# Performance work log

Hardware: AMD Instinct MI355X
Metric: run time of the kernel (lower is better)

The kernel has to match this reference:

```python
import jax, jax.numpy as jnp
import numpy as np

B, N, D = 16, 32768, 256
E, H, K, T = 512, 8, 512, 16  # text_embed_dim, nhead, top_k, num_defect_tokens
LN_EPS = 1e-5


def setup_inputs() -> dict:
    key = jax.random.key(0)
    ks = jax.random.split(key, 8)
    sc = 0.02
    return {
        "per_point_features": jax.random.normal(ks[0], (B, N, D), jnp.float32),
        "outlier_scores": jax.random.normal(ks[1], (B, N, 1), jnp.float32),
        "proj_w": jax.random.normal(ks[2], (E, D), jnp.float32) * sc,
        "proj_b": jnp.zeros((E,), jnp.float32),
        "in_proj_w": jax.random.normal(ks[3], (3 * E, E), jnp.float32) * sc,
        "in_proj_b": jnp.zeros((3 * E,), jnp.float32),
        "out_proj_w": jax.random.normal(ks[4], (E, E), jnp.float32) * sc,
        "out_proj_b": jnp.zeros((E,), jnp.float32),
        "ln_g": jnp.ones((E,), jnp.float32),
        "ln_b": jnp.zeros((E,), jnp.float32),
        "ffn_w": jax.random.normal(ks[5], (E, E), jnp.float32) * sc,
        "ffn_b": jnp.zeros((E,), jnp.float32),
    }


def _layernorm(x, g, b):
    mu = jnp.mean(x, axis=-1, keepdims=True)
    var = jnp.mean(jnp.square(x - mu), axis=-1, keepdims=True)
    return (x - mu) * jax.lax.rsqrt(var + LN_EPS) * g + b


def reference(per_point_features, outlier_scores, proj_w, proj_b,
              in_proj_w, in_proj_b, out_proj_w, out_proj_b,
              ln_g, ln_b, ffn_w, ffn_b):
    # top-k select + gather
    scores = outlier_scores[..., 0]                       # [B, N]
    _, idx = jax.lax.top_k(scores, K)                     # [B, K]
    feats = jnp.take_along_axis(per_point_features, idx[:, :, None], axis=1)  # [B, K, D]
    # linear projection to text embed dim
    x = feats @ proj_w.T + proj_b                         # [B, K, E]
    # multi-head self-attention (torch nn.MultiheadAttention semantics)
    qkv = x @ in_proj_w.T + in_proj_b                     # [B, K, 3E]
    q, k, v = jnp.split(qkv, 3, axis=-1)
    dh = E // H
    q = q.reshape(B, K, H, dh)
    k = k.reshape(B, K, H, dh)
    v = v.reshape(B, K, H, dh)
    logits = jnp.einsum("bqhd,bkhd->bhqk", q, k) / np.sqrt(dh).astype(np.float32)
    attn = jax.nn.softmax(logits, axis=-1)
    o = jnp.einsum("bhqk,bkhd->bqhd", attn, v).reshape(B, K, E)
    o = o @ out_proj_w.T + out_proj_b
    # residual + layernorm
    y = _layernorm(x + o, ln_g, ln_b)
    # FFN (linear + exact GELU) with residual
    y = y + jax.nn.gelu(y @ ffn_w.T + ffn_b, approximate=False)
    return y[:, :T, :]                                    # [B, T, E]
```

## Files before the change

### kernel.cpp

```cpp
#include <hip/hip_runtime.h>
#include <hip/hip_bf16.h>
#include <math.h>

#define PB 16
#define PN 32768
#define PD 256
#define PE 512
#define PH 8
#define PK 512
#define PT 16
#define DH 64

typedef __attribute__((ext_vector_type(8))) short bf16x8;
typedef __attribute__((ext_vector_type(4))) float f32x4;

__global__ __launch_bounds__(512) void topk_kernel(const float* __restrict__ scores,
                                                   int* __restrict__ sorted_idx) {
    const int b = blockIdx.x;
    const int tid = threadIdx.x;
    const int NT = 512;
    const float* s = scores + (size_t)b * PN;

    __shared__ unsigned int hist[256];
    __shared__ unsigned int sh_prefix;
    __shared__ int sh_remaining;
    __shared__ unsigned int sh_cnt_gt, sh_cnt_eq;
    __shared__ unsigned long long comp[PK];
    __shared__ unsigned int eq_idx[PK];

    unsigned int prefix = 0;
    int remaining = PK;
    for (int shift = 24; shift >= 0; shift -= 8) {
        for (int i = tid; i < 256; i += NT) hist[i] = 0;
        __syncthreads();
        for (int i = tid; i < PN; i += NT) {
            unsigned int u = __float_as_uint(s[i]);
            u = (u & 0x80000000u) ? ~u : (u | 0x80000000u);
            bool ok = (shift == 24) || ((u >> (shift + 8)) == prefix);
            if (ok) atomicAdd(&hist[(u >> shift) & 0xFFu], 1u);
        }
        __syncthreads();
        if (tid == 0) {
            int cum = 0;
            int d = 255;
            for (; d >= 0; --d) {
                cum += (int)hist[d];
                if (cum >= remaining) break;
            }
            sh_remaining = remaining - (cum - (int)hist[d]);
            sh_prefix = (prefix << 8) | (unsigned)d;
        }
        __syncthreads();
        prefix = sh_prefix;
        remaining = sh_remaining;
        __syncthreads();
    }
    const unsigned int TKEY = prefix;

    if (tid == 0) { sh_cnt_gt = 0; sh_cnt_eq = 0; }
    __syncthreads();
    for (int i = tid; i < PN; i += NT) {
        unsigned int u = __float_as_uint(s[i]);
        u = (u & 0x80000000u) ? ~u : (u | 0x80000000u);
        if (u > TKEY) {
            unsigned p = atomicAdd(&sh_cnt_gt, 1u);
            comp[p] = ((unsigned long long)u << 32) | (unsigned int)(~(unsigned)i);
        } else if (u == TKEY) {
            unsigned p = atomicAdd(&sh_cnt_eq, 1u);
            if (p < PK) eq_idx[p] = (unsigned)i;
        }
    }
    __syncthreads();
    const int cnt_gt = (int)sh_cnt_gt;
    const int need_eq = PK - cnt_gt;
    const int ec = (int)sh_cnt_eq < PK ? (int)sh_cnt_eq : PK;
    if (tid == 0) {
        for (int j = 0; j < need_eq; ++j) {
            unsigned mv = 0xFFFFFFFFu; int mb = 0;
            for (int i2 = 0; i2 < ec; ++i2)
                if (eq_idx[i2] < mv) { mv = eq_idx[i2]; mb = i2; }
            comp[cnt_gt + j] = ((unsigned long long)TKEY << 32) | (unsigned int)(~mv);
            eq_idx[mb] = 0xFFFFFFFFu;
        }
    }
    __syncthreads();

    for (unsigned ksz = 2; ksz <= PK; ksz <<= 1) {
        for (unsigned j = ksz >> 1; j > 0; j >>= 1) {
            unsigned i = (unsigned)tid;
            unsigned ixj = i ^ j;
            if (ixj > i && i < PK) {
                unsigned long long a = comp[i], c = comp[ixj];
                bool sw = ((i & ksz) == 0) ? (a < c) : (a > c);
                if (sw) { comp[i] = c; comp[ixj] = a; }
            }
            __syncthreads();
        }
    }
    if (tid < PK)
        sorted_idx[b * PK + tid] = (int)(~(unsigned int)(comp[tid] & 0xFFFFFFFFull));
}

__global__ void gather_cast_kernel(const float* __restrict__ feats,
                                   const int* __restrict__ sidx,
                                   __hip_bfloat16* __restrict__ Ag) {
    const int row = blockIdx.x;
    const int b = row >> 9;
    const int src = sidx[row];
    const float* p = feats + ((size_t)b * PN + (size_t)src) * PD;
    __hip_bfloat16* q = Ag + (size_t)row * PD;
    for (int i = threadIdx.x; i < PD; i += blockDim.x)
        q[i] = __float2bfloat16(p[i]);
}

__global__ void cast_f32_bf16_kernel(const float* __restrict__ src,
                                     __hip_bfloat16* __restrict__ dst, int n) {
    int i = blockIdx.x * blockDim.x + threadIdx.x;
    if (i < n) dst[i] = __float2bfloat16(src[i]);
}

__global__ __launch_bounds__(256) void gemm_bt_bf16_kernel(
    const short* __restrict__ A, const short* __restrict__ Bm,
    const float* __restrict__ bias,
    float* __restrict__ C32, __hip_bfloat16* __restrict__ C16,
    int M, int N, int Kd) {
    const int tid = threadIdx.x;
    const int wave = tid >> 6;
    const int lane = tid & 63;
    const int m0 = blockIdx.x * 128 + (wave >> 1) * 64;
    const int n0 = blockIdx.y * 128 + (wave & 1) * 64;
    const int mrow = lane & 15;
    const int quad = lane >> 4;

    f32x4 acc[4][4] = {};
    for (int k0 = 0; k0 < Kd; k0 += 32) {
        const int kk = k0 + quad * 8;
        bf16x8 a[4], bf[4];
#pragma unroll
        for (int i = 0; i < 4; ++i)
            a[i] = *(const bf16x8*)(A + (size_t)(m0 + i * 16 + mrow) * Kd + kk);
#pragma unroll
        for (int i = 0; i < 4; ++i)
            bf[i] = *(const bf16x8*)(Bm + (size_t)(n0 + i * 16 + mrow) * Kd + kk);
#pragma unroll
        for (int i = 0; i < 4; ++i)
#pragma unroll
            for (int j = 0; j < 4; ++j)
                acc[i][j] = __builtin_amdgcn_mfma_f32_16x16x32_bf16(a[i], bf[j], acc[i][j], 0, 0, 0);
    }
#pragma unroll
    for (int i = 0; i < 4; ++i)
#pragma unroll
        for (int j = 0; j < 4; ++j)
#pragma unroll
            for (int r = 0; r < 4; ++r) {
                int row = m0 + i * 16 + quad * 4 + r;
                int col = n0 + j * 16 + mrow;
                float v = acc[i][j][r] + bias[col];
                if (C32) C32[(size_t)row * N + col] = v;
                if (C16) C16[(size_t)row * N + col] = __float2bfloat16(v);
            }
}

__global__ void extract_xq_kernel(const float* __restrict__ x, float* __restrict__ xq) {
    const int r = blockIdx.x;
    const int b = r >> 4, t = r & 15;
    const float* src = x + ((size_t)b * PK + t) * PE;
    float* dst = xq + (size_t)r * PE;
    for (int i = threadIdx.x; i < PE; i += blockDim.x) dst[i] = src[i];
}

__global__ __launch_bounds__(256) void sgemm_bt_kernel(
    const float* __restrict__ A, const float* __restrict__ Bm,
    const float* __restrict__ bias, float* __restrict__ C,
    int M, int N, int Kd) {
    __shared__ float As[32][33];
    __shared__ float Bs[32][33];
    const int tid = threadIdx.x;
    const int m0 = blockIdx.x * 32, n0 = blockIdx.y * 32;
    const int tx = tid & 15, ty = tid >> 4;
    float acc00 = 0, acc01 = 0, acc10 = 0, acc11 = 0;
    for (int k0 = 0; k0 < Kd; k0 += 32) {
        for (int e = tid; e < 1024; e += 256) {
            int r = e >> 5, c = e & 31;
            As[r][c] = A[(size_t)(m0 + r) * Kd + k0 + c];
            Bs[r][c] = Bm[(size_t)(n0 + r) * Kd + k0 + c];
        }
        __syncthreads();
#pragma unroll
        for (int kk = 0; kk < 32; ++kk) {
            float a0 = As[ty * 2][kk], a1 = As[ty * 2 + 1][kk];
            float b0 = Bs[tx * 2][kk], b1 = Bs[tx * 2 + 1][kk];
            acc00 += a0 * b0; acc01 += a0 * b1;
            acc10 += a1 * b0; acc11 += a1 * b1;
        }
        __syncthreads();
    }
    float bc0 = bias[n0 + tx * 2], bc1 = bias[n0 + tx * 2 + 1];
    C[(size_t)(m0 + ty * 2) * N + n0 + tx * 2]         = acc00 + bc0;
    C[(size_t)(m0 + ty * 2) * N + n0 + tx * 2 + 1]     = acc01 + bc1;
    C[(size_t)(m0 + ty * 2 + 1) * N + n0 + tx * 2]     = acc10 + bc0;
    C[(size_t)(m0 + ty * 2 + 1) * N + n0 + tx * 2 + 1] = acc11 + bc1;
}

__global__ __launch_bounds__(256) void attn_kernel(
    const float* __restrict__ qb, const __hip_bfloat16* __restrict__ kv,
    float* __restrict__ ob) {
    const int bh = blockIdx.x;
    const int b = bh >> 3, h = bh & 7;
    const int tid = threadIdx.x;
    __shared__ float qs[PT][DH + 1];
    __shared__ float ls[PT][PK + 1];

    for (int i = tid; i < PT * DH; i += 256) {
        int t = i >> 6, d = i & 63;
        qs[t][d] = qb[(size_t)(b * PT + t) * PE + h * DH + d];
    }
    __syncthreads();

    const int t = tid >> 4;
    const int ko = tid & 15;
    for (int k = ko; k < PK; k += 16) {
        const __hip_bfloat16* kp = kv + (size_t)(b * PK + k) * (2 * PE) + h * DH;
        float acc = 0;
#pragma unroll 8
        for (int d = 0; d < DH; ++d) acc += qs[t][d] * __bfloat162float(kp[d]);
        ls[t][k] = acc * 0.125f;
    }
    float m = -1e30f;
    for (int k = ko; k < PK; k += 16) m = fmaxf(m, ls[t][k]);
#pragma unroll
    for (int s = 8; s >= 1; s >>= 1) m = fmaxf(m, __shfl_xor(m, s, 16));
    float sum = 0;
    for (int k = ko; k < PK; k += 16) {
        float e = __expf(ls[t][k] - m);
        ls[t][k] = e;
        sum += e;
    }
#pragma unroll
    for (int s = 8; s >= 1; s >>= 1) sum += __shfl_xor(sum, s, 16);
    const float inv = 1.0f / sum;

    const int dv = tid & 15;
    float o0 = 0, o1 = 0, o2 = 0, o3 = 0;
    for (int k = 0; k < PK; ++k) {
        float w = ls[t][k];
        const __hip_bfloat16* vp = kv + (size_t)(b * PK + k) * (2 * PE) + PE + h * DH;
        o0 += w * __bfloat162float(vp[dv]);
        o1 += w * __bfloat162float(vp[dv + 16]);
        o2 += w * __bfloat162float(vp[dv + 32]);
        o3 += w * __bfloat162float(vp[dv + 48]);
    }
    float* orow = ob + (size_t)(b * PT + t) * PE + h * DH;
    orow[dv]      = o0 * inv;
    orow[dv + 16] = o1 * inv;
    orow[dv + 32] = o2 * inv;
    orow[dv + 48] = o3 * inv;
}

__global__ __launch_bounds__(256) void ln_kernel(
    const float* __restrict__ xq, const float* __restrict__ o2,
    const float* __restrict__ g, const float* __restrict__ bb,
    float* __restrict__ y) {
    const int r = blockIdx.x;
    const int tid = threadIdx.x;
    __shared__ float red[4], red2[4];
    float v0 = xq[(size_t)r * PE + tid] + o2[(size_t)r * PE + tid];
    float v1 = xq[(size_t)r * PE + 256 + tid] + o2[(size_t)r * PE + 256 + tid];
    float s = v0 + v1;
#pragma unroll
    for (int sh = 32; sh >= 1; sh >>= 1) s += __shfl_xor(s, sh, 64);
    if ((tid & 63) == 0) red[tid >> 6] = s;
    __syncthreads();
    float mean = (red[0] + red[1] + red[2] + red[3]) * (1.0f / 512.0f);
    float d0 = v0 - mean, d1 = v1 - mean;
    float sq = d0 * d0 + d1 * d1;
#pragma unroll
    for (int sh = 32; sh >= 1; sh >>= 1) sq += __shfl_xor(sq, sh, 64);
    if ((tid & 63) == 0) red2[tid >> 6] = sq;
    __syncthreads();
    float var = (red2[0] + red2[1] + red2[2] + red2[3]) * (1.0f / 512.0f);
    float rs = rsqrtf(var + 1e-5f);
    y[(size_t)r * PE + tid]       = d0 * rs * g[tid] + bb[tid];
    y[(size_t)r * PE + 256 + tid] = d1 * rs * g[tid + 256] + bb[tid + 256];
}

__global__ void gelu_res_kernel(const float* __restrict__ y,
                                const float* __restrict__ z,
                                float* __restrict__ out, int n) {
    int i = blockIdx.x * blockDim.x + threadIdx.x;
    if (i < n) {
        float zz = z[i];
        float gl = 0.5f * zz * (1.0f + erff(zz * 0.7071067811865475f));
        out[i] = y[i] + gl;
    }
}

extern "C" void kernel_launch(void* const* d_in, const int* in_sizes, int n_in,
                              void* d_out, int out_size, void* d_ws, size_t ws_size,
                              hipStream_t stream) {
    const float* feats  = (const float*)d_in[0];
    const float* scores = (const float*)d_in[1];
    const float* proj_w = (const float*)d_in[2];
    const float* proj_b = (const float*)d_in[3];
    const float* in_w   = (const float*)d_in[4];
    const float* in_b   = (const float*)d_in[5];
    const float* out_w  = (const float*)d_in[6];
    const float* out_b  = (const float*)d_in[7];
    const float* ln_g   = (const float*)d_in[8];
    const float* ln_b   = (const float*)d_in[9];
    const float* ffn_w  = (const float*)d_in[10];
    const float* ffn_b  = (const float*)d_in[11];
    float* out = (float*)d_out;

    char* p = (char*)d_ws;
    auto alloc = [&](size_t bytes) {
        void* r = (void*)p;
        p += (bytes + 255) & ~(size_t)255;
        return r;
    };
    int* sidx             = (int*)alloc((size_t)PB * PK * 4);
    __hip_bfloat16* Ag    = (__hip_bfloat16*)alloc((size_t)PB * PK * PD * 2);
    __hip_bfloat16* Wp16  = (__hip_bfloat16*)alloc((size_t)PE * PD * 2);
    __hip_bfloat16* Wkv16 = (__hip_bfloat16*)alloc((size_t)2 * PE * PE * 2);
    float* x32            = (float*)alloc((size_t)PB * PK * PE * 4);
    __hip_bfloat16* x16   = (__hip_bfloat16*)alloc((size_t)PB * PK * PE * 2);
    __hip_bfloat16* kv16  = (__hip_bfloat16*)alloc((size_t)PB * PK * 2 * PE * 2);
    float* xq             = (float*)alloc((size_t)PB * PT * PE * 4);
    float* qb             = (float*)alloc((size_t)PB * PT * PE * 4);
    float* ob             = (float*)alloc((size_t)PB * PT * PE * 4);
    float* o2             = (float*)alloc((size_t)PB * PT * PE * 4);
    float* yb             = (float*)alloc((size_t)PB * PT * PE * 4);
    float* zb             = (float*)alloc((size_t)PB * PT * PE * 4);
    if ((size_t)(p - (char*)d_ws) > ws_size) return;

    topk_kernel<<<PB, 512, 0, stream>>>(scores, sidx);
    gather_cast_kernel<<<PB * PK, 64, 0, stream>>>(feats, sidx, Ag);
    cast_f32_bf16_kernel<<<(PE * PD + 255) / 256, 256, 0, stream>>>(proj_w, Wp16, PE * PD);
    cast_f32_bf16_kernel<<<(2 * PE * PE + 255) / 256, 256, 0, stream>>>(in_w + (size_t)PE * PE, Wkv16, 2 * PE * PE);
    gemm_bt_bf16_kernel<<<dim3(64, 4), 256, 0, stream>>>(
        (const short*)Ag, (const short*)Wp16, proj_b, x32, x16, PB * PK, PE, PD);
    gemm_bt_bf16_kernel<<<dim3(64, 8), 256, 0, stream>>>(
        (const short*)x16, (const short*)Wkv16, in_b + PE, nullptr, kv16,
        PB * PK, 2 * PE, PE);
    extract_xq_kernel<<<PB * PT, 256, 0, stream>>>(x32, xq);
    sgemm_bt_kernel<<<dim3(8, 16), 256, 0, stream>>>(xq, in_w, in_b, qb, PB * PT, PE, PE);
    attn_kernel<<<PB * PH, 256, 0, stream>>>(qb, kv16, ob);
    sgemm_bt_kernel<<<dim3(8, 16), 256, 0, stream>>>(ob, out_w, out_b, o2, PB * PT, PE, PE);
    ln_kernel<<<PB * PT, 256, 0, stream>>>(xq, o2, ln_g, ln_b, yb);
    sgemm_bt_kernel<<<dim3(8, 16), 256, 0, stream>>>(yb, ffn_w, ffn_b, zb, PB * PT, PE, PE);
    gelu_res_kernel<<<(PB * PT * PE + 255) / 256, 256, 0, stream>>>(yb, zb, out, PB * PT * PE);
}
```

Before: 966.1 us.

## Vectorize loads, fuse casts, xq extraction and GELU epilogue, drop fp32 x buffer

Top-k histogram and selection passes now read scores as float4. The gather now uses one wave per row with float4 loads, and the two weight casts are merged into one vectorized kernel. The projection GEMM writes the first 16 token rows straight to xq instead of storing a full fp32 x and extracting it later. GELU plus residual moves into the FFN sgemm epilogue, and the attention kernel uses vectorized bf16 loads. Together these cut launches and memory traffic, with the main cost likely in the top-k kernel, which runs with only 16 blocks.

```diff
diff --git a/kernel.cpp b/kernel.cpp
--- a/kernel.cpp
+++ b/kernel.cpp
@@ -14,6 +14,14 @@
 typedef __attribute__((ext_vector_type(8))) short bf16x8;
 typedef __attribute__((ext_vector_type(4))) float f32x4;
 
+__device__ __forceinline__ unsigned short f2bf(float f) {
+    __hip_bfloat16 h = __float2bfloat16(f);
+    return *(unsigned short*)&h;
+}
+__device__ __forceinline__ float b2f(unsigned short u) {
+    return __uint_as_float(((unsigned int)u) << 16);
+}
+
 __global__ __launch_bounds__(512) void topk_kernel(const float* __restrict__ scores,
                                                    int* __restrict__ sorted_idx) {
     const int b = blockIdx.x;
@@ -33,11 +41,16 @@
     for (int shift = 24; shift >= 0; shift -= 8) {
         for (int i = tid; i < 256; i += NT) hist[i] = 0;
         __syncthreads();
-        for (int i = tid; i < PN; i += NT) {
-            unsigned int u = __float_as_uint(s[i]);
-            u = (u & 0x80000000u) ? ~u : (u | 0x80000000u);
-            bool ok = (shift == 24) || ((u >> (shift + 8)) == prefix);
-            if (ok) atomicAdd(&hist[(u >> shift) & 0xFFu], 1u);
+        for (int i = tid * 4; i < PN; i += NT * 4) {
+            float4 f = *(const float4*)(s + i);
+            const float* fp = (const float*)&f;
+#pragma unroll
+            for (int j = 0; j < 4; ++j) {
+                unsigned int u = __float_as_uint(fp[j]);
+                u = (u & 0x80000000u) ? ~u : (u | 0x80000000u);
+                bool ok = (shift == 24) || ((u >> (shift + 8)) == prefix);
+                if (ok) atomicAdd(&hist[(u >> shift) & 0xFFu], 1u);
+            }
         }
         __syncthreads();
         if (tid == 0) {
@@ -59,15 +72,20 @@
 
     if (tid == 0) { sh_cnt_gt = 0; sh_cnt_eq = 0; }
     __syncthreads();
-    for (int i = tid; i < PN; i += NT) {
-        unsigned int u = __float_as_uint(s[i]);
-        u = (u & 0x80000000u) ? ~u : (u | 0x80000000u);
-        if (u > TKEY) {
-            unsigned p = atomicAdd(&sh_cnt_gt, 1u);
-            comp[p] = ((unsigned long long)u << 32) | (unsigned int)(~(unsigned)i);
-        } else if (u == TKEY) {
-            unsigned p = atomicAdd(&sh_cnt_eq, 1u);
-            if (p < PK) eq_idx[p] = (unsigned)i;
+    for (int i = tid * 4; i < PN; i += NT * 4) {
+        float4 f = *(const float4*)(s + i);
+        const float* fp = (const float*)&f;
+#pragma unroll
+        for (int j = 0; j < 4; ++j) {
+            unsigned int u = __float_as_uint(fp[j]);
+            u = (u & 0x80000000u) ? ~u : (u | 0x80000000u);
+            if (u > TKEY) {
+                unsigned p = atomicAdd(&sh_cnt_gt, 1u);
+                comp[p] = ((unsigned long long)u << 32) | (unsigned int)(~(unsigned)(i + j));
+            } else if (u == TKEY) {
+                unsigned p = atomicAdd(&sh_cnt_eq, 1u);
+                if (p < PK) eq_idx[p] = (unsigned)(i + j);
+            }
         }
     }
     __syncthreads();
@@ -101,28 +119,41 @@
         sorted_idx[b * PK + tid] = (int)(~(unsigned int)(comp[tid] & 0xFFFFFFFFull));
 }
 
-__global__ void gather_cast_kernel(const float* __restrict__ feats,
-                                   const int* __restrict__ sidx,
-                                   __hip_bfloat16* __restrict__ Ag) {
-    const int row = blockIdx.x;
+__global__ __launch_bounds__(256) void gather_cast_kernel(const float* __restrict__ feats,
+                                                          const int* __restrict__ sidx,
+                                                          __hip_bfloat16* __restrict__ Ag) {
+    const int row = blockIdx.x * 4 + (threadIdx.x >> 6);
+    const int lane = threadIdx.x & 63;
     const int b = row >> 9;
     const int src = sidx[row];
-    const float* p = feats + ((size_t)b * PN + (size_t)src) * PD;
-    __hip_bfloat16* q = Ag + (size_t)row * PD;
-    for (int i = threadIdx.x; i < PD; i += blockDim.x)
-        q[i] = __float2bfloat16(p[i]);
-}
-
-__global__ void cast_f32_bf16_kernel(const float* __restrict__ src,
-                                     __hip_bfloat16* __restrict__ dst, int n) {
-    int i = blockIdx.x * blockDim.x + threadIdx.x;
-    if (i < n) dst[i] = __float2bfloat16(src[i]);
+    float4 f = *(const float4*)(feats + ((size_t)b * PN + (size_t)src) * PD + lane * 4);
+    ushort4 u;
+    u.x = f2bf(f.x); u.y = f2bf(f.y); u.z = f2bf(f.z); u.w = f2bf(f.w);
+    *(ushort4*)((unsigned short*)Ag + (size_t)row * PD + lane * 4) = u;
+}
+
+__global__ __launch_bounds__(256) void cast_weights_kernel(
+    const float* __restrict__ proj_w, const float* __restrict__ kv_w,
+    __hip_bfloat16* __restrict__ Wp16, __hip_bfloat16* __restrict__ Wkv16) {
+    const int n1 = PE * PD / 4;
+    const int n2 = 2 * PE * PE / 4;
+    int i = blockIdx.x * 256 + threadIdx.x;
+    const float4* src;
+    unsigned short* dst;
+    int off;
+    if (i < n1) { src = (const float4*)proj_w; dst = (unsigned short*)Wp16; off = i; }
+    else if (i < n1 + n2) { src = (const float4*)kv_w; dst = (unsigned short*)Wkv16; off = i - n1; }
+    else return;
+    float4 f = src[off];
+    ushort4 u;
+    u.x = f2bf(f.x); u.y = f2bf(f.y); u.z = f2bf(f.z); u.w = f2bf(f.w);
+    *(ushort4*)(dst + (size_t)off * 4) = u;
 }
 
 __global__ __launch_bounds__(256) void gemm_bt_bf16_kernel(
     const short* __restrict__ A, const short* __restrict__ Bm,
     const float* __restrict__ bias,
-    float* __restrict__ C32, __hip_bfloat16* __restrict__ C16,
+    __hip_bfloat16* __restrict__ C16, float* __restrict__ Xq,
     int M, int N, int Kd) {
     const int tid = threadIdx.x;
     const int wave = tid >> 6;
@@ -157,23 +188,22 @@
                 int row = m0 + i * 16 + quad * 4 + r;
                 int col = n0 + j * 16 + mrow;
                 float v = acc[i][j][r] + bias[col];
-                if (C32) C32[(size_t)row * N + col] = v;
-                if (C16) C16[(size_t)row * N + col] = __float2bfloat16(v);
-            }
-}
-
-__global__ void extract_xq_kernel(const float* __restrict__ x, float* __restrict__ xq) {
-    const int r = blockIdx.x;
-    const int b = r >> 4, t = r & 15;
-    const float* src = x + ((size_t)b * PK + t) * PE;
-    float* dst = xq + (size_t)r * PE;
-    for (int i = threadIdx.x; i < PE; i += blockDim.x) dst[i] = src[i];
+                if (C16) {
+                    __hip_bfloat16 hv = __float2bfloat16(v);
+                    ((__hip_bfloat16*)C16)[(size_t)row * N + col] = hv;
+                }
+                if (Xq) {
+                    int t = row & (PK - 1);
+                    if (t < PT)
+                        Xq[((size_t)(row >> 9) * PT + t) * N + col] = v;
+                }
+            }
 }
 
 __global__ __launch_bounds__(256) void sgemm_bt_kernel(
     const float* __restrict__ A, const float* __restrict__ Bm,
-    const float* __restrict__ bias, float* __restrict__ C,
-    int M, int N, int Kd) {
+    const float* __restrict__ bias, const float* __restrict__ resid,
+    float* __restrict__ C, int M, int N, int Kd) {
     __shared__ float As[32][33];
     __shared__ float Bs[32][33];
     const int tid = threadIdx.x;
@@ -197,10 +227,17 @@
         __syncthreads();
     }
     float bc0 = bias[n0 + tx * 2], bc1 = bias[n0 + tx * 2 + 1];
-    C[(size_t)(m0 + ty * 2) * N + n0 + tx * 2]         = acc00 + bc0;
-    C[(size_t)(m0 + ty * 2) * N + n0 + tx * 2 + 1]     = acc01 + bc1;
-    C[(size_t)(m0 + ty * 2 + 1) * N + n0 + tx * 2]     = acc10 + bc0;
-    C[(size_t)(m0 + ty * 2 + 1) * N + n0 + tx * 2 + 1] = acc11 + bc1;
+    float v00 = acc00 + bc0, v01 = acc01 + bc1, v10 = acc10 + bc0, v11 = acc11 + bc1;
+    size_t i00 = (size_t)(m0 + ty * 2) * N + n0 + tx * 2;
+    size_t i10 = (size_t)(m0 + ty * 2 + 1) * N + n0 + tx * 2;
+    if (resid) {
+        v00 = resid[i00]     + 0.5f * v00 * (1.0f + erff(v00 * 0.7071067811865475f));
+        v01 = resid[i00 + 1] + 0.5f * v01 * (1.0f + erff(v01 * 0.7071067811865475f));
+        v10 = resid[i10]     + 0.5f * v10 * (1.0f + erff(v10 * 0.7071067811865475f));
+        v11 = resid[i10 + 1] + 0.5f * v11 * (1.0f + erff(v11 * 0.7071067811865475f));
+    }
+    C[i00] = v00; C[i00 + 1] = v01;
+    C[i10] = v10; C[i10 + 1] = v11;
 }
 
 __global__ __launch_bounds__(256) void attn_kernel(
@@ -209,22 +246,29 @@
     const int bh = blockIdx.x;
     const int b = bh >> 3, h = bh & 7;
     const int tid = threadIdx.x;
-    __shared__ float qs[PT][DH + 1];
+    __shared__ float qs[PT][DH + 4];
     __shared__ float ls[PT][PK + 1];
 
-    for (int i = tid; i < PT * DH; i += 256) {
-        int t = i >> 6, d = i & 63;
-        qs[t][d] = qb[(size_t)(b * PT + t) * PE + h * DH + d];
+    {
+        int i4 = tid * 4;
+        int t = i4 >> 6, d = i4 & 63;
+        float4 f = *(const float4*)(qb + (size_t)(b * PT + t) * PE + h * DH + d);
+        qs[t][d] = f.x; qs[t][d + 1] = f.y; qs[t][d + 2] = f.z; qs[t][d + 3] = f.w;
     }
     __syncthreads();
 
     const int t = tid >> 4;
     const int ko = tid & 15;
     for (int k = ko; k < PK; k += 16) {
-        const __hip_bfloat16* kp = kv + (size_t)(b * PK + k) * (2 * PE) + h * DH;
+        const ushort4* kp = (const ushort4*)((const unsigned short*)kv +
+                             (size_t)(b * PK + k) * (2 * PE) + h * DH);
         float acc = 0;
-#pragma unroll 8
-        for (int d = 0; d < DH; ++d) acc += qs[t][d] * __bfloat162float(kp[d]);
+#pragma unroll
+        for (int c = 0; c < 16; ++c) {
+            ushort4 vv = kp[c];
+            acc += qs[t][c * 4 + 0] * b2f(vv.x) + qs[t][c * 4 + 1] * b2f(vv.y)
+                 + qs[t][c * 4 + 2] * b2f(vv.z) + qs[t][c * 4 + 3] * b2f(vv.w);
+        }
         ls[t][k] = acc * 0.125f;
     }
     float m = -1e30f;
@@ -241,21 +285,19 @@
     for (int s = 8; s >= 1; s >>= 1) sum += __shfl_xor(sum, s, 16);
     const float inv = 1.0f / sum;
 
-    const int dv = tid & 15;
+    const int d0 = (tid & 15) * 4;
+    const unsigned short* vbase = (const unsigned short*)kv +
+                                  (size_t)(b * PK) * (2 * PE) + PE + h * DH + d0;
     float o0 = 0, o1 = 0, o2 = 0, o3 = 0;
+#pragma unroll 4
     for (int k = 0; k < PK; ++k) {
         float w = ls[t][k];
-        const __hip_bfloat16* vp = kv + (size_t)(b * PK + k) * (2 * PE) + PE + h * DH;
-        o0 += w * __bfloat162float(vp[dv]);
-        o1 += w * __bfloat162float(vp[dv + 16]);
-        o2 += w * __bfloat162float(vp[dv + 32]);
-        o3 += w * __bfloat162float(vp[dv + 48]);
-    }
-    float* orow = ob + (size_t)(b * PT + t) * PE + h * DH;
-    orow[dv]      = o0 * inv;
-    orow[dv + 16] = o1 * inv;
-    orow[dv + 32] = o2 * inv;
-    orow[dv + 48] = o3 * inv;
+        ushort4 vv = *(const ushort4*)(vbase + (size_t)k * (2 * PE));
+        o0 += w * b2f(vv.x); o1 += w * b2f(vv.y);
+        o2 += w * b2f(vv.z); o3 += w * b2f(vv.w);
+    }
+    float4 o; o.x = o0 * inv; o.y = o1 * inv; o.z = o2 * inv; o.w = o3 * inv;
+    *(float4*)(ob + (size_t)(b * PT + t) * PE + h * DH + d0) = o;
 }
 
 __global__ __launch_bounds__(256) void ln_kernel(
@@ -283,17 +325,6 @@
     float rs = rsqrtf(var + 1e-5f);
     y[(size_t)r * PE + tid]       = d0 * rs * g[tid] + bb[tid];
     y[(size_t)r * PE + 256 + tid] = d1 * rs * g[tid + 256] + bb[tid + 256];
-}
-
-__global__ void gelu_res_kernel(const float* __restrict__ y,
-                                const float* __restrict__ z,
-                                float* __restrict__ out, int n) {
-    int i = blockIdx.x * blockDim.x + threadIdx.x;
-    if (i < n) {
-        float zz = z[i];
-        float gl = 0.5f * zz * (1.0f + erff(zz * 0.7071067811865475f));
-        out[i] = y[i] + gl;
-    }
 }
 
 extern "C" void kernel_launch(void* const* d_in, const int* in_sizes, int n_in,
@@ -323,7 +354,6 @@
     __hip_bfloat16* Ag    = (__hip_bfloat16*)alloc((size_t)PB * PK * PD * 2);
     __hip_bfloat16* Wp16  = (__hip_bfloat16*)alloc((size_t)PE * PD * 2);
     __hip_bfloat16* Wkv16 = (__hip_bfloat16*)alloc((size_t)2 * PE * PE * 2);
-    float* x32            = (float*)alloc((size_t)PB * PK * PE * 4);
     __hip_bfloat16* x16   = (__hip_bfloat16*)alloc((size_t)PB * PK * PE * 2);
     __hip_bfloat16* kv16  = (__hip_bfloat16*)alloc((size_t)PB * PK * 2 * PE * 2);
     float* xq             = (float*)alloc((size_t)PB * PT * PE * 4);
@@ -331,23 +361,23 @@
     float* ob             = (float*)alloc((size_t)PB * PT * PE * 4);
     float* o2             = (float*)alloc((size_t)PB * PT * PE * 4);
     float* yb             = (float*)alloc((size_t)PB * PT * PE * 4);
-    float* zb             = (float*)alloc((size_t)PB * PT * PE * 4);
     if ((size_t)(p - (char*)d_ws) > ws_size) return;
 
     topk_kernel<<<PB, 512, 0, stream>>>(scores, sidx);
-    gather_cast_kernel<<<PB * PK, 64, 0, stream>>>(feats, sidx, Ag);
-    cast_f32_bf16_kernel<<<(PE * PD + 255) / 256, 256, 0, stream>>>(proj_w, Wp16, PE * PD);
-    cast_f32_bf16_kernel<<<(2 * PE * PE + 255) / 256, 256, 0, stream>>>(in_w + (size_t)PE * PE, Wkv16, 2 * PE * PE);
+    gather_cast_kernel<<<PB * PK / 4, 256, 0, stream>>>(feats, sidx, Ag);
+    {
+        int nvec = (PE * PD + 2 * PE * PE) / 4;
+        cast_weights_kernel<<<(nvec + 255) / 256, 256, 0, stream>>>(
+            proj_w, in_w + (size_t)PE * PE, Wp16, Wkv16);
+    }
     gemm_bt_bf16_kernel<<<dim3(64, 4), 256, 0, stream>>>(
-        (const short*)Ag, (const short*)Wp16, proj_b, x32, x16, PB * PK, PE, PD);
+        (const short*)Ag, (const short*)Wp16, proj_b, x16, xq, PB * PK, PE, PD);
     gemm_bt_bf16_kernel<<<dim3(64, 8), 256, 0, stream>>>(
-        (const short*)x16, (const short*)Wkv16, in_b + PE, nullptr, kv16,
+        (const short*)x16, (const short*)Wkv16, in_b + PE, kv16, nullptr,
         PB * PK, 2 * PE, PE);
-    extract_xq_kernel<<<PB * PT, 256, 0, stream>>>(x32, xq);
-    sgemm_bt_kernel<<<dim3(8, 16), 256, 0, stream>>>(xq, in_w, in_b, qb, PB * PT, PE, PE);
+    sgemm_bt_kernel<<<dim3(8, 16), 256, 0, stream>>>(xq, in_w, in_b, nullptr, qb, PB * PT, PE, PE);
     attn_kernel<<<PB * PH, 256, 0, stream>>>(qb, kv16, ob);
-    sgemm_bt_kernel<<<dim3(8, 16), 256, 0, stream>>>(ob, out_w, out_b, o2, PB * PT, PE, PE);
+    sgemm_bt_kernel<<<dim3(8, 16), 256, 0, stream>>>(ob, out_w, out_b, nullptr, o2, PB * PT, PE, PE);
     ln_kernel<<<PB * PT, 256, 0, stream>>>(xq, o2, ln_g, ln_b, yb);
-    sgemm_bt_kernel<<<dim3(8, 16), 256, 0, stream>>>(yb, ffn_w, ffn_b, zb, PB * PT, PE, PE);
-    gelu_res_kernel<<<(PB * PT * PE + 255) / 256, 256, 0, stream>>>(yb, zb, out, PB * PT * PE);
-}
+    sgemm_bt_kernel<<<dim3(8, 16), 256, 0, stream>>>(yb, ffn_w, ffn_b, yb, out, PB * PT, PE, PE);
+}
```

After: 909.0 us. -5.9%, faster.
